# Kernel optimization log

Measured on AMD Instinct MI355X. Metric: run time of the kernel, lower is better.

## Reference

```python
import jax, jax.numpy as jnp
import numpy as np

B, T, C, R = 4, 2048, 2048, 256


def setup_inputs() -> dict:
    key = jax.random.key(0)
    ks = jax.random.split(key, 12)
    s = 0.02
    return {
        "x": jax.random.normal(ks[0], (B, T, C), dtype=jnp.float32),
        "h_state": jnp.zeros((B, C), dtype=jnp.float32),
        "ln_gamma": jnp.ones((C,), dtype=jnp.float32),
        "ln_beta": jnp.zeros((C,), dtype=jnp.float32),
        "wq_a": jax.random.normal(ks[1], (C, R), dtype=jnp.float32) * s,
        "wq_b": jax.random.normal(ks[2], (R, C), dtype=jnp.float32) * s,
        "wk_a": jax.random.normal(ks[3], (C, R), dtype=jnp.float32) * s,
        "wk_b": jax.random.normal(ks[4], (R, C), dtype=jnp.float32) * s,
        "wv_a": jax.random.normal(ks[5], (C, R), dtype=jnp.float32) * s,
        "wv_b": jax.random.normal(ks[6], (R, C), dtype=jnp.float32) * s,
        "out_w": jax.random.normal(ks[7], (C, C), dtype=jnp.float32) * s,
        "out_b": jnp.zeros((C,), dtype=jnp.float32),
        "time_decay": jnp.full((C,), -0.5, dtype=jnp.float32),
    }


def _layernorm(x, gamma, beta, eps=1e-5):
    mu = jnp.mean(x, axis=-1, keepdims=True)
    var = jnp.var(x, axis=-1, keepdims=True)
    return (x - mu) * jax.lax.rsqrt(var + eps) * gamma + beta


def reference(x, h_state, ln_gamma, ln_beta, wq_a, wq_b, wk_a, wk_b, wv_a, wv_b, out_w, out_b, time_decay):
    b, t, c = x.shape
    xn = _layernorm(x, ln_gamma, ln_beta)
    # token shift: mix current with previous token
    x_shift = jnp.concatenate([jnp.zeros((b, 1, c), xn.dtype), xn[:, :-1, :]], axis=1)
    mix = 0.5 * xn + 0.5 * x_shift
    # low-rank projections: (B,T,C) @ (C,R) @ (R,C)
    q = jnp.einsum('btc,cr,rd->btd', mix, wq_a, wq_b)
    k = jnp.einsum('btc,cr,rd->btd', mix, wk_a, wk_b)
    v = jnp.einsum('btc,cr,rd->btd', mix, wv_a, wv_b)
    decay = jnp.exp(-jnp.exp(time_decay))  # (C,)

    kv = (k * v).transpose(1, 0, 2)          # (T,B,C)
    sq = jax.nn.sigmoid(q).transpose(1, 0, 2)  # (T,B,C)

    def step(h, inp):
        kv_t, sq_t = inp
        h = decay * h + kv_t
        return h, sq_t * h

    h_final, ys = jax.lax.scan(step, h_state, (kv, sq))
    out = ys.transpose(1, 0, 2)               # (B,T,C)
    out = jnp.einsum('btc,dc->btd', out, out_w) + out_b
    return out, h_final
```

## Files before the change

kernel.cpp:

```cpp
#include <hip/hip_runtime.h>


typedef __attribute__((ext_vector_type(8))) __bf16 bf16x8;
typedef __attribute__((ext_vector_type(4))) float f32x4;

static constexpr int Bb = 4, Tt = 2048, Cc = 2048, Rr = 256;
static constexpr int Mrows = Bb * Tt;
static constexpr int NCH = 32, CLEN = 64;

__device__ __forceinline__ unsigned short f2bf(float f) {
  union { float f; unsigned u; } a; a.f = f;
  unsigned r = (a.u + 0x7FFFu + ((a.u >> 16) & 1u)) >> 16;
  return (unsigned short)r;
}
__device__ __forceinline__ float bf2f(unsigned short h) {
  union { unsigned u; float f; } a; a.u = ((unsigned)h) << 16;
  return a.f;
}

__device__ __forceinline__ void gload16(const void* g, void* l) {
  __builtin_amdgcn_global_load_lds(
      (const __attribute__((address_space(1))) void*)g,
      (__attribute__((address_space(3))) void*)l, 16, 0, 0);
}

__global__ void prep_weights(const float* __restrict__ wqa, const float* __restrict__ wka,
                             const float* __restrict__ wva, const float* __restrict__ wqb,
                             const float* __restrict__ wkb, const float* __restrict__ wvb,
                             const float* __restrict__ ow,  const float* __restrict__ td,
                             unsigned short* __restrict__ waT, unsigned short* __restrict__ wbT,
                             unsigned short* __restrict__ owT, float* __restrict__ decay,
                             float* __restrict__ decayL) {
  const int g = blockIdx.x * blockDim.x + threadIdx.x;
  const int stride = gridDim.x * blockDim.x;
  for (int i = g; i < 3 * Rr * Cc; i += stride) {
    int c = i & (Cc - 1); int jj = i >> 11; int p = jj >> 8; int r = jj & (Rr - 1);
    const float* w = (p == 0) ? wqa : ((p == 1) ? wka : wva);
    waT[i] = f2bf(w[(size_t)c * Rr + r]);
  }
  for (int i = g; i < 3 * Cc * Rr; i += stride) {
    int r = i & (Rr - 1); int d = (i >> 8) & (Cc - 1); int p = i >> 19;
    const float* w = (p == 0) ? wqb : ((p == 1) ? wkb : wvb);
    wbT[i] = f2bf(w[(size_t)r * Cc + d]);
  }
  for (int i = g; i < Cc * Cc; i += stride) owT[i] = f2bf(ow[i]);
  for (int i = g; i < Cc; i += stride) {
    float e = expf(td[i]);
    decay[i] = expf(-e);
    decayL[i] = expf(-(float)CLEN * e);
  }
}

__global__ __launch_bounds__(256) void lnmix_kernel(
    const float* __restrict__ x, const float* __restrict__ gamma,
    const float* __restrict__ beta, unsigned short* __restrict__ mix) {
  const int m = blockIdx.x;
  const int t = m & (Tt - 1);
  const float* xr = x + (size_t)m * Cc;
  float s0 = 0.f, q0 = 0.f, s1 = 0.f, q1 = 0.f;
  float4 cur[2], prv[2];
#pragma unroll
  for (int r = 0; r < 2; ++r) {
    int i = threadIdx.x + r * 256;
    float4 v = ((const float4*)xr)[i];
    cur[r] = v;
    s0 += v.x + v.y + v.z + v.w;
    q0 += v.x * v.x + v.y * v.y + v.z * v.z + v.w * v.w;
  }
  if (t > 0) {
    const float* xp = xr - Cc;
#pragma unroll
    for (int r = 0; r < 2; ++r) {
      int i = threadIdx.x + r * 256;
      float4 v = ((const float4*)xp)[i];
      prv[r] = v;
      s1 += v.x + v.y + v.z + v.w;
      q1 += v.x * v.x + v.y * v.y + v.z * v.z + v.w * v.w;
    }
  }
#pragma unroll
  for (int off = 32; off; off >>= 1) {
    s0 += __shfl_down(s0, off); q0 += __shfl_down(q0, off);
    s1 += __shfl_down(s1, off); q1 += __shfl_down(q1, off);
  }
  __shared__ float red[4][4];
  __shared__ float bc[4];
  if ((threadIdx.x & 63) == 0) {
    int w = threadIdx.x >> 6;
    red[w][0] = s0; red[w][1] = q0; red[w][2] = s1; red[w][3] = q1;
  }
  __syncthreads();
  if (threadIdx.x == 0) {
    float a0 = 0, b0 = 0, a1 = 0, b1 = 0;
    for (int w = 0; w < 4; ++w) { a0 += red[w][0]; b0 += red[w][1]; a1 += red[w][2]; b1 += red[w][3]; }
    float mu0 = a0 * (1.f / Cc);
    bc[0] = mu0; bc[1] = rsqrtf(b0 * (1.f / Cc) - mu0 * mu0 + 1e-5f);
    float mu1 = a1 * (1.f / Cc);
    bc[2] = mu1; bc[3] = rsqrtf(b1 * (1.f / Cc) - mu1 * mu1 + 1e-5f);
  }
  __syncthreads();
  const float mu0 = bc[0], rs0 = bc[1], mu1 = bc[2], rs1 = bc[3];
#pragma unroll
  for (int r = 0; r < 2; ++r) {
    int i = threadIdx.x + r * 256;
    float4 g = ((const float4*)gamma)[i];
    float4 bb = ((const float4*)beta)[i];
    float4 v = cur[r];
    float mx = (v.x - mu0) * rs0 * g.x + bb.x;
    float my = (v.y - mu0) * rs0 * g.y + bb.y;
    float mz = (v.z - mu0) * rs0 * g.z + bb.z;
    float mw = (v.w - mu0) * rs0 * g.w + bb.w;
    if (t > 0) {
      float4 u = prv[r];
      mx = 0.5f * (mx + (u.x - mu1) * rs1 * g.x + bb.x);
      my = 0.5f * (my + (u.y - mu1) * rs1 * g.y + bb.y);
      mz = 0.5f * (mz + (u.z - mu1) * rs1 * g.z + bb.z);
      mw = 0.5f * (mw + (u.w - mu1) * rs1 * g.w + bb.w);
    } else {
      mx *= 0.5f; my *= 0.5f; mz *= 0.5f; mw *= 0.5f;
    }
    ushort4 o;
    o.x = f2bf(mx); o.y = f2bf(my); o.z = f2bf(mz); o.w = f2bf(mw);
    ((ushort4*)mix)[(size_t)m * 512 + i] = o;
  }
}

template <bool STORE_BF16, bool ADD_BIAS>
__global__ __launch_bounds__(512, 2) void gemm_pipe(
    const unsigned short* __restrict__ A0p, long lda, long aStrideP,
    const unsigned short* __restrict__ B0p, long ldb, long bStrideP,
    void* c0, void* c1, void* c2, long ldc, int K,
    const float* __restrict__ bias, int nbx, int nby) {
  __shared__ unsigned short lds[8 * 8192];
  const int tid = threadIdx.x;
  const int nwg = gridDim.x;
  const int id = blockIdx.x;
  const int q = nwg >> 3;
  const int swz = (id & 7) * q + (id >> 3);
  const int per = nbx * nby;
  const int p = swz / per;
  const int r2 = swz - p * per;
  const int nblk = r2 / nby;
  const int mblk = r2 - nblk * nby;
  const unsigned short* A  = A0p + (long)p * aStrideP;
  const unsigned short* Bt = B0p + (long)p * bStrideP;
  void* Cout = (p == 0) ? c0 : (p == 1 ? c1 : c2);
  const long m0 = (long)mblk * 256, n0 = (long)nblk * 256;

  const int lane = tid & 63, wid = tid >> 6;
  const int wm = wid >> 2, wn = wid & 3;
  const int fr = lane & 15, fq = lane >> 4;

  const int srow = tid >> 2;
  const int s_src = (tid & 3) ^ ((tid >> 3) & 3);
  const unsigned short* Ag = A + (m0 + srow) * lda + s_src * 8;

  const int swzs = fq ^ ((fr >> 1) & 3);
  const unsigned short* aBase = &lds[(wm * 128 + fr) * 32 + swzs * 8];

  const unsigned short* Bgp = Bt + (n0 + wn * 64 + fr) * ldb + fq * 8;

  f32x4 acc[8][4];
#pragma unroll
  for (int i = 0; i < 8; ++i)
#pragma unroll
    for (int j = 0; j < 4; ++j) acc[i][j] = (f32x4){0.f, 0.f, 0.f, 0.f};

  const int NT = K >> 5;
  const int NP = NT >> 1;

  auto stageA = [&](int t) {
    unsigned short* d = &lds[(t & 7) * 8192 + tid * 8];
    const long kt = (long)t * 32;
    gload16(Ag + kt, d);
    gload16(Ag + 128 * lda + kt, d + 4096);
  };
  bf16x8 bcur[4], bnxt[4];
  auto loadB = [&](bf16x8* dst, int t) {
    const long co = (long)t * 32;
#pragma unroll
    for (int j = 0; j < 4; ++j)
      dst[j] = *(const bf16x8*)(Bgp + (long)(j * 16) * ldb + co);
  };

  stageA(0); stageA(1); stageA(2); stageA(3);
  loadB(bcur, 0);

  for (int pr = 0; pr < NP; ++pr) {
    const int t0 = 2 * pr, t1 = 2 * pr + 1;
    asm volatile("s_waitcnt vmcnt(8)" ::: "memory");
    __builtin_amdgcn_s_barrier();
    __builtin_amdgcn_sched_barrier(0);

    {
      const unsigned short* ab = aBase + (t0 & 7) * 8192;
      bf16x8 af[8];
#pragma unroll
      for (int i = 0; i < 8; ++i) af[i] = *(const bf16x8*)(ab + i * 512);
      loadB(bnxt, t1);
      if (t0 + 4 < NT) { stageA(t0 + 4); stageA(t0 + 5); }
      __builtin_amdgcn_s_setprio(1);
#pragma unroll
      for (int i = 0; i < 8; ++i)
#pragma unroll
        for (int j = 0; j < 4; ++j)
          acc[i][j] = __builtin_amdgcn_mfma_f32_16x16x32_bf16(af[i], bcur[j], acc[i][j], 0, 0, 0);
      __builtin_amdgcn_s_setprio(0);
    }
    {
      const unsigned short* ab = aBase + (t1 & 7) * 8192;
      bf16x8 af[8];
#pragma unroll
      for (int i = 0; i < 8; ++i) af[i] = *(const bf16x8*)(ab + i * 512);
      if (t1 + 1 < NT) loadB(bcur, t1 + 1);
      __builtin_amdgcn_s_setprio(1);
#pragma unroll
      for (int i = 0; i < 8; ++i)
#pragma unroll
        for (int j = 0; j < 4; ++j)
          acc[i][j] = __builtin_amdgcn_mfma_f32_16x16x32_bf16(af[i], bnxt[j], acc[i][j], 0, 0, 0);
      __builtin_amdgcn_s_setprio(0);
    }
  }

#pragma unroll
  for (int j = 0; j < 4; ++j) {
    const long col = n0 + wn * 64 + j * 16 + fr;
    const float bv = ADD_BIAS ? bias[col] : 0.0f;
#pragma unroll
    for (int i = 0; i < 8; ++i) {
      const long row0 = m0 + wm * 128 + i * 16 + fq * 4;
#pragma unroll
      for (int r = 0; r < 4; ++r) {
        float val = acc[i][j][r] + bv;
        if (STORE_BF16)
          ((unsigned short*)Cout)[(row0 + r) * ldc + col] = f2bf(val);
        else
          ((float*)Cout)[(row0 + r) * ldc + col] = val;
      }
    }
  }
}

__global__ void addcvt_kernel(const float* __restrict__ p0, const float* __restrict__ p1,
                              unsigned short* __restrict__ o, int n4) {
  for (int i = blockIdx.x * blockDim.x + threadIdx.x; i < n4; i += gridDim.x * blockDim.x) {
    float4 a = ((const float4*)p0)[i];
    float4 b = ((const float4*)p1)[i];
    ushort4 r;
    r.x = f2bf(a.x + b.x); r.y = f2bf(a.y + b.y);
    r.z = f2bf(a.z + b.z); r.w = f2bf(a.w + b.w);
    ((ushort4*)o)[i] = r;
  }
}

__global__ void scan_phaseA(const unsigned short* __restrict__ k, const unsigned short* __restrict__ v,
                            const float* __restrict__ decay, float* __restrict__ hend) {
  const int g = blockIdx.x * 256 + threadIdx.x;
  const int c = g & (Cc - 1);
  const int j = (g >> 11) & (NCH - 1);
  const int b = g >> 16;
  const float d = decay[c];
  size_t base = ((size_t)(b * Tt + j * CLEN)) * Cc + c;
  float h = 0.f;
#pragma unroll 8
  for (int s = 0; s < CLEN; ++s) {
    size_t idx = base + (size_t)s * Cc;
    float kv = bf2f(k[idx]) * bf2f(v[idx]);
    h = fmaf(d, h, kv);
  }
  hend[(size_t)(b * NCH + j) * Cc + c] = h;
}

__global__ void scan_combine(const float* __restrict__ hend, const float* __restrict__ h0,
                             const float* __restrict__ decayL, float* __restrict__ Hin,
                             float* __restrict__ hfinal) {
  const int g = blockIdx.x * 256 + threadIdx.x;
  const int c = g & (Cc - 1);
  float H = h0[g];
  const float dl = decayL[c];
  const int b = g >> 11;
  for (int j = 0; j < NCH; ++j) {
    size_t idx = (size_t)(b * NCH + j) * Cc + c;
    Hin[idx] = H;
    H = fmaf(dl, H, hend[idx]);
  }
  hfinal[g] = H;
}

__global__ void scan_phaseB(const unsigned short* __restrict__ q, const unsigned short* __restrict__ k,
                            const unsigned short* __restrict__ v, const float* __restrict__ decay,
                            const float* __restrict__ Hin, unsigned short* __restrict__ ys) {
  const int g = blockIdx.x * 256 + threadIdx.x;
  const int c = g & (Cc - 1);
  const int j = (g >> 11) & (NCH - 1);
  const int b = g >> 16;
  const float d = decay[c];
  float h = Hin[(size_t)(b * NCH + j) * Cc + c];
  size_t base = ((size_t)(b * Tt + j * CLEN)) * Cc + c;
#pragma unroll 4
  for (int s = 0; s < CLEN; ++s) {
    size_t idx = base + (size_t)s * Cc;
    float kv = bf2f(k[idx]) * bf2f(v[idx]);
    h = fmaf(d, h, kv);
    float qq = bf2f(q[idx]);
    float sg = 1.f / (1.f + expf(-qq));
    ys[idx] = f2bf(sg * h);
  }
}

extern "C" void kernel_launch(void* const* d_in, const int* in_sizes, int n_in,
                              void* d_out, int out_size, void* d_ws, size_t ws_size,
                              hipStream_t stream) {
  const float* x   = (const float*)d_in[0];
  const float* h0  = (const float*)d_in[1];
  const float* gam = (const float*)d_in[2];
  const float* bet = (const float*)d_in[3];
  const float* wqa = (const float*)d_in[4];
  const float* wqb = (const float*)d_in[5];
  const float* wka = (const float*)d_in[6];
  const float* wkb = (const float*)d_in[7];
  const float* wva = (const float*)d_in[8];
  const float* wvb = (const float*)d_in[9];
  const float* ow  = (const float*)d_in[10];
  const float* ob  = (const float*)d_in[11];
  const float* td  = (const float*)d_in[12];
  float* out = (float*)d_out;

  char* ws = (char*)d_ws;
  unsigned short* waT   = (unsigned short*)(ws + 0);
  unsigned short* wbT   = (unsigned short*)(ws + 3145728);
  unsigned short* owT   = (unsigned short*)(ws + 6291456);
  float*          decay = (float*)(ws + 14680064);
  float*          decayL= (float*)(ws + 14688256);
  unsigned short* mixb  = (unsigned short*)(ws + 14761984);
  unsigned short* tmp   = (unsigned short*)(ws + 48316416);
  unsigned short* vp    = (unsigned short*)(ws + 60899328);
  float*          hend  = (float*)(ws + 94453760);
  float*          Hin   = (float*)(ws + 95502336);
  float* P0 = (float*)d_out;
  float* P1 = P0 + (size_t)Mrows * 768;
  unsigned short* qp = (unsigned short*)d_out;
  unsigned short* kp = qp + (size_t)Mrows * Cc;
  float* hfinal = out + (size_t)Mrows * Cc;
  unsigned short* ysb = mixb;

  prep_weights<<<1024, 256, 0, stream>>>(wqa, wka, wva, wqb, wkb, wvb, ow, td,
                                         waT, wbT, owT, decay, decayL);
  lnmix_kernel<<<Mrows, 256, 0, stream>>>(x, gam, bet, mixb);

  gemm_pipe<false, false><<<192, 512, 0, stream>>>(
      mixb, Cc, 1024, waT, Cc, 1024,
      P0, P1, nullptr, 768, 1024, nullptr, 3, 32);
  addcvt_kernel<<<1024, 256, 0, stream>>>(P0, P1, tmp, Mrows * 768 / 4);

  gemm_pipe<true, false><<<8 * 32 * 3, 512, 0, stream>>>(
      tmp, 768, 256, wbT, Rr, (long)Cc * Rr,
      qp, kp, vp, Cc, Rr, nullptr, 8, 32);

  scan_phaseA<<<(Bb * NCH * Cc) / 256, 256, 0, stream>>>(kp, vp, decay, hend);
  scan_combine<<<(Bb * Cc) / 256, 256, 0, stream>>>(hend, h0, decayL, Hin, hfinal);
  scan_phaseB<<<(Bb * NCH * Cc) / 256, 256, 0, stream>>>(qp, kp, vp, decay, Hin, ysb);

  gemm_pipe<false, true><<<8 * 32, 512, 0, stream>>>(
      ysb, Cc, 0, owT, Cc, 0,
      out, out, out, Cc, Cc, ob, 8, 32);
}
```

Baseline: 300.2 us.

## Stage B tiles through LDS with 8-phase double-buffered GEMM pipeline

Reworks the bf16 MFMA GEMM so both A and B tiles are staged into LDS with direct global-to-LDS loads, where before B was read straight from global memory into registers. The K loop now takes 64-wide steps split into four sub-phases over a two-slot buffer, with barriers and vmcnt waits between phases. Launch bounds drop to one workgroup per CU and the tile index order changes so neighbouring blocks walk along N within the same M block. The goal is to share B across waves and reduce redundant global traffic, at the cost of more barriers and lower occupancy.

```diff
diff --git a/kernel.cpp b/kernel.cpp
--- a/kernel.cpp
+++ b/kernel.cpp
@@ -126,22 +126,22 @@
 }
 
 template <bool STORE_BF16, bool ADD_BIAS>
-__global__ __launch_bounds__(512, 2) void gemm_pipe(
+__global__ __launch_bounds__(512, 1) void gemm8p(
     const unsigned short* __restrict__ A0p, long lda, long aStrideP,
     const unsigned short* __restrict__ B0p, long ldb, long bStrideP,
     void* c0, void* c1, void* c2, long ldc, int K,
     const float* __restrict__ bias, int nbx, int nby) {
-  __shared__ unsigned short lds[8 * 8192];
+  __shared__ unsigned short lds[65536];
   const int tid = threadIdx.x;
   const int nwg = gridDim.x;
   const int id = blockIdx.x;
-  const int q = nwg >> 3;
-  const int swz = (id & 7) * q + (id >> 3);
+  const int qq = nwg >> 3;
+  const int swz = (id & 7) * qq + (id >> 3);
   const int per = nbx * nby;
   const int p = swz / per;
   const int r2 = swz - p * per;
-  const int nblk = r2 / nby;
-  const int mblk = r2 - nblk * nby;
+  const int mblk = r2 / nbx;
+  const int nblk = r2 - mblk * nbx;
   const unsigned short* A  = A0p + (long)p * aStrideP;
   const unsigned short* Bt = B0p + (long)p * bStrideP;
   void* Cout = (p == 0) ? c0 : (p == 1 ? c1 : c2);
@@ -153,12 +153,14 @@
 
   const int srow = tid >> 2;
   const int s_src = (tid & 3) ^ ((tid >> 3) & 3);
-  const unsigned short* Ag = A + (m0 + srow) * lda + s_src * 8;
+  const unsigned short* AgH0 = A + (m0 + srow) * lda + s_src * 8;
+  const unsigned short* AgH1 = A + (m0 + 128 + srow) * lda + s_src * 8;
+  const unsigned short* BgH0 = Bt + (n0 + srow) * ldb + s_src * 8;
+  const unsigned short* BgH1 = Bt + (n0 + 128 + srow) * ldb + s_src * 8;
 
   const int swzs = fq ^ ((fr >> 1) & 3);
-  const unsigned short* aBase = &lds[(wm * 128 + fr) * 32 + swzs * 8];
-
-  const unsigned short* Bgp = Bt + (n0 + wn * 64 + fr) * ldb + fq * 8;
+  const int aOff = wm * 8192 + fr * 32 + swzs * 8;
+  const int bOff = 16384 + (wn >> 1) * 8192 + ((wn & 1) * 64 + fr) * 32 + swzs * 8;
 
   f32x4 acc[8][4];
 #pragma unroll
@@ -166,60 +168,104 @@
 #pragma unroll
     for (int j = 0; j < 4; ++j) acc[i][j] = (f32x4){0.f, 0.f, 0.f, 0.f};
 
-  const int NT = K >> 5;
-  const int NP = NT >> 1;
-
-  auto stageA = [&](int t) {
-    unsigned short* d = &lds[(t & 7) * 8192 + tid * 8];
-    const long kt = (long)t * 32;
-    gload16(Ag + kt, d);
-    gload16(Ag + 128 * lda + kt, d + 4096);
+  const int NT = K >> 6;
+
+  auto stageA2 = [&](int tt, int kh) {
+    unsigned short* d = &lds[((tt & 1) << 15) + (kh << 12) + tid * 8];
+    const long co = (long)tt * 64 + kh * 32;
+    gload16(AgH0 + co, d);
+    gload16(AgH1 + co, d + 8192);
   };
-  bf16x8 bcur[4], bnxt[4];
-  auto loadB = [&](bf16x8* dst, int t) {
-    const long co = (long)t * 32;
-#pragma unroll
-    for (int j = 0; j < 4; ++j)
-      dst[j] = *(const bf16x8*)(Bgp + (long)(j * 16) * ldb + co);
+  auto stageB2 = [&](int tt, int kh) {
+    unsigned short* d = &lds[((tt & 1) << 15) + 16384 + (kh << 12) + tid * 8];
+    const long co = (long)tt * 64 + kh * 32;
+    gload16(BgH0 + co, d);
+    gload16(BgH1 + co, d + 8192);
   };
 
-  stageA(0); stageA(1); stageA(2); stageA(3);
-  loadB(bcur, 0);
-
-  for (int pr = 0; pr < NP; ++pr) {
-    const int t0 = 2 * pr, t1 = 2 * pr + 1;
-    asm volatile("s_waitcnt vmcnt(8)" ::: "memory");
-    __builtin_amdgcn_s_barrier();
-    __builtin_amdgcn_sched_barrier(0);
+  stageA2(0, 0); stageB2(0, 0);
+  stageA2(0, 1); stageB2(0, 1);
+  stageA2(1, 0); stageB2(1, 0);
+  asm volatile("s_waitcnt vmcnt(8)" ::: "memory");
+  __builtin_amdgcn_s_barrier();
+  __builtin_amdgcn_sched_barrier(0);
+
+  for (int t = 0; t < NT; ++t) {
+    const int P = (t & 1) << 15;
+    const unsigned short* ap = &lds[P + aOff];
+    const unsigned short* bp = &lds[P + bOff];
 
     {
-      const unsigned short* ab = aBase + (t0 & 7) * 8192;
-      bf16x8 af[8];
-#pragma unroll
-      for (int i = 0; i < 8; ++i) af[i] = *(const bf16x8*)(ab + i * 512);
-      loadB(bnxt, t1);
-      if (t0 + 4 < NT) { stageA(t0 + 4); stageA(t0 + 5); }
+      bf16x8 af[4], bf[4];
+#pragma unroll
+      for (int j = 0; j < 4; ++j) bf[j] = *(const bf16x8*)(bp + j * 512);
+#pragma unroll
+      for (int i = 0; i < 4; ++i) af[i] = *(const bf16x8*)(ap + i * 512);
+      if (t + 1 < NT) stageA2(t + 1, 1);
       __builtin_amdgcn_s_setprio(1);
 #pragma unroll
-      for (int i = 0; i < 8; ++i)
+      for (int i = 0; i < 4; ++i)
 #pragma unroll
         for (int j = 0; j < 4; ++j)
-          acc[i][j] = __builtin_amdgcn_mfma_f32_16x16x32_bf16(af[i], bcur[j], acc[i][j], 0, 0, 0);
+          acc[i][j] = __builtin_amdgcn_mfma_f32_16x16x32_bf16(af[i], bf[j], acc[i][j], 0, 0, 0);
       __builtin_amdgcn_s_setprio(0);
+      __builtin_amdgcn_s_barrier();
+      __builtin_amdgcn_sched_barrier(0);
     }
     {
-      const unsigned short* ab = aBase + (t1 & 7) * 8192;
-      bf16x8 af[8];
-#pragma unroll
-      for (int i = 0; i < 8; ++i) af[i] = *(const bf16x8*)(ab + i * 512);
-      if (t1 + 1 < NT) loadB(bcur, t1 + 1);
+      bf16x8 af[4], bf[4];
+#pragma unroll
+      for (int j = 0; j < 4; ++j) bf[j] = *(const bf16x8*)(bp + j * 512);
+#pragma unroll
+      for (int i = 0; i < 4; ++i) af[i] = *(const bf16x8*)(ap + 2048 + i * 512);
+      if (t + 1 < NT) stageB2(t + 1, 1);
       __builtin_amdgcn_s_setprio(1);
 #pragma unroll
-      for (int i = 0; i < 8; ++i)
+      for (int i = 0; i < 4; ++i)
 #pragma unroll
         for (int j = 0; j < 4; ++j)
-          acc[i][j] = __builtin_amdgcn_mfma_f32_16x16x32_bf16(af[i], bnxt[j], acc[i][j], 0, 0, 0);
+          acc[4 + i][j] = __builtin_amdgcn_mfma_f32_16x16x32_bf16(af[i], bf[j], acc[4 + i][j], 0, 0, 0);
       __builtin_amdgcn_s_setprio(0);
+      if (t + 1 < NT) asm volatile("s_waitcnt vmcnt(8)" ::: "memory");
+      else            asm volatile("s_waitcnt vmcnt(0)" ::: "memory");
+      __builtin_amdgcn_s_barrier();
+      __builtin_amdgcn_sched_barrier(0);
+    }
+    {
+      bf16x8 af[4], bf[4];
+#pragma unroll
+      for (int j = 0; j < 4; ++j) bf[j] = *(const bf16x8*)(bp + 4096 + j * 512);
+#pragma unroll
+      for (int i = 0; i < 4; ++i) af[i] = *(const bf16x8*)(ap + 4096 + i * 512);
+      if (t + 2 < NT) stageA2(t + 2, 0);
+      __builtin_amdgcn_s_setprio(1);
+#pragma unroll
+      for (int i = 0; i < 4; ++i)
+#pragma unroll
+        for (int j = 0; j < 4; ++j)
+          acc[i][j] = __builtin_amdgcn_mfma_f32_16x16x32_bf16(af[i], bf[j], acc[i][j], 0, 0, 0);
+      __builtin_amdgcn_s_setprio(0);
+      __builtin_amdgcn_s_barrier();
+      __builtin_amdgcn_sched_barrier(0);
+    }
+    {
+      bf16x8 af[4], bf[4];
+#pragma unroll
+      for (int j = 0; j < 4; ++j) bf[j] = *(const bf16x8*)(bp + 4096 + j * 512);
+#pragma unroll
+      for (int i = 0; i < 4; ++i) af[i] = *(const bf16x8*)(ap + 4096 + 2048 + i * 512);
+      if (t + 2 < NT) stageB2(t + 2, 0);
+      __builtin_amdgcn_s_setprio(1);
+#pragma unroll
+      for (int i = 0; i < 4; ++i)
+#pragma unroll
+        for (int j = 0; j < 4; ++j)
+          acc[4 + i][j] = __builtin_amdgcn_mfma_f32_16x16x32_bf16(af[i], bf[j], acc[4 + i][j], 0, 0, 0);
+      __builtin_amdgcn_s_setprio(0);
+      if (t + 2 < NT)      asm volatile("s_waitcnt vmcnt(8)" ::: "memory");
+      else if (t + 1 < NT) asm volatile("s_waitcnt vmcnt(4)" ::: "memory");
+      __builtin_amdgcn_s_barrier();
+      __builtin_amdgcn_sched_barrier(0);
     }
   }
 
@@ -349,12 +395,12 @@
                                          waT, wbT, owT, decay, decayL);
   lnmix_kernel<<<Mrows, 256, 0, stream>>>(x, gam, bet, mixb);
 
-  gemm_pipe<false, false><<<192, 512, 0, stream>>>(
+  gemm8p<false, false><<<192, 512, 0, stream>>>(
       mixb, Cc, 1024, waT, Cc, 1024,
       P0, P1, nullptr, 768, 1024, nullptr, 3, 32);
   addcvt_kernel<<<1024, 256, 0, stream>>>(P0, P1, tmp, Mrows * 768 / 4);
 
-  gemm_pipe<true, false><<<8 * 32 * 3, 512, 0, stream>>>(
+  gemm8p<true, false><<<768, 512, 0, stream>>>(
       tmp, 768, 256, wbT, Rr, (long)Cc * Rr,
       qp, kp, vp, Cc, Rr, nullptr, 8, 32);
 
@@ -362,7 +408,7 @@
   scan_combine<<<(Bb * Cc) / 256, 256, 0, stream>>>(hend, h0, decayL, Hin, hfinal);
   scan_phaseB<<<(Bb * NCH * Cc) / 256, 256, 0, stream>>>(qp, kp, vp, decay, Hin, ysb);
 
-  gemm_pipe<false, true><<<8 * 32, 512, 0, stream>>>(
+  gemm8p<false, true><<<256, 512, 0, stream>>>(
       ysb, Cc, 0, owT, Cc, 0,
       out, out, out, Cc, Cc, ob, 8, 32);
 }
```

Measured after the change: 265.7 us. 1.13x faster.
